# Performance work log

Hardware: AMD Instinct MI355X
Metric: run time of the kernel (lower is better)

Reference implementation:

```python
import jax, jax.numpy as jnp
import numpy as np

K = 16  # kNN size (self included)
R = 4   # upsampling ratio


def _knn(pts, k):
    # pts: (B,N,3) -> idx (B,N,k); smallest distance first, so idx[:,:,0] is self
    sq = jnp.sum(pts * pts, axis=-1)
    d = sq[:, :, None] - 2.0 * jnp.einsum('bnd,bmd->bnm', pts, pts) + sq[:, None, :]
    _, idx = jax.lax.top_k(-d, k)
    return idx


def _gather(feats, idx):
    # feats (B,N,C), idx (B,N,k) -> (B,N,k,C)
    return jax.vmap(lambda f, i: f[i])(feats, idx)


def _conv1d(x, w, b):  # pointwise Conv1d: x (B,C,N)
    return jnp.einsum('oc,bcn->bon', w, x) + b[None, :, None]


def _conv2d(x, w, b):  # pointwise Conv2d: x (B,C,N,K)
    return jnp.einsum('oc,bcnk->bonk', w, x) + b[None, :, None, None]


def setup_inputs() -> dict:
    key = jax.random.key(0)
    ks = jax.random.split(key, 16)
    B, N = 2, 8192
    w = lambda k, s: jax.random.normal(k, s, jnp.float32) * 0.1
    return {
        'x': jax.random.normal(ks[0], (B, 3, N), jnp.float32),
        'mlp1_w1': w(ks[1], (32, 3)), 'mlp1_b1': jnp.zeros((32,), jnp.float32),
        'mlp1_w2': w(ks[2], (64, 32)), 'mlp1_b2': jnp.zeros((64,), jnp.float32),
        'mlp2_w1': w(ks[3], (32, 9)), 'mlp2_b1': jnp.zeros((32,), jnp.float32),
        'mlp3_w1': w(ks[4], (128, 96)), 'mlp3_b1': jnp.zeros((128,), jnp.float32),
        'mlp3_w2': w(ks[5], (12, 128)), 'mlp3_b2': jnp.zeros((12,), jnp.float32),
        'att_w1': w(ks[6], (128, 64)), 'att_b1': jnp.zeros((128,), jnp.float32),
        'att_w2': w(ks[7], (64, 128)), 'att_b2': jnp.zeros((64,), jnp.float32),
    }


def reference(x, mlp1_w1, mlp1_b1, mlp1_w2, mlp1_b2, mlp2_w1, mlp2_b1,
              mlp3_w1, mlp3_b1, mlp3_w2, mlp3_b2,
              att_w1, att_b1, att_w2, att_b2):
    B, C, N = x.shape
    pts = jnp.transpose(x, (0, 2, 1))                     # (B,N,3)
    idx = _knn(jax.lax.stop_gradient(pts), K)             # (B,N,K)

    # local 3x3 covariance features -> (B,9,N)
    nb = _gather(pts, idx)                                # (B,N,K,3)
    c = nb - jnp.mean(nb, axis=2, keepdims=True)
    cov = jnp.einsum('bnki,bnkj->bnij', c, c) / K         # (B,N,3,3)
    cov_feat = jnp.transpose(cov.reshape(B, N, 9), (0, 2, 1))

    # mlp1: 3 -> 32 -> 64, relu on both (last_act=True)
    f1 = jax.nn.relu(_conv1d(jax.nn.relu(_conv1d(x, mlp1_w1, mlp1_b1)), mlp1_w2, mlp1_b2))

    # gather neighbor features (exclude self) and form relative features
    fk = _gather(jnp.transpose(f1, (0, 2, 1)), idx[:, :, 1:])   # (B,N,K-1,64)
    f_knn = jnp.transpose(fk, (0, 3, 1, 2)) - f1[:, :, :, None]  # (B,64,N,K-1)

    # attention MLP (2D): 64 -> 128 -> 64, softmax over neighbor axis
    h = jax.nn.relu(_conv2d(f_knn, att_w1, att_b1))
    w = jax.nn.softmax(_conv2d(h, att_w2, att_b2), axis=-1)
    f_agg = jnp.sum(w * f_knn, axis=-1)                   # (B,64,N)

    # mlp2: 9 -> 32 with relu
    f_cov = jax.nn.relu(_conv1d(cov_feat, mlp2_w1, mlp2_b1))     # (B,32,N)

    f = jnp.concatenate([f_agg, f_cov], axis=1)           # (B,96,N)
    g = _conv1d(jax.nn.relu(_conv1d(f, mlp3_w1, mlp3_b1)), mlp3_w2, mlp3_b2)  # (B,3R,N)

    return jnp.tile(x, (1, 1, R)) + 0.15 * g.reshape(B, -1, R * N)
```

## Files before the change

### kernel.cpp

```cpp
#include <hip/hip_runtime.h>

#define BB 2
#define NN 8192
#define KK 16
#define QPB 64
#define PRE2 128
#define SLICE 512
#define STASH 32
#define EPSF 0.02f
typedef unsigned long long ull;
typedef unsigned short ushort;
#define KINF 0xFFFFFFFFFFFFFFFFULL
#define BFONE 0x3F80

typedef __attribute__((ext_vector_type(8))) short short8;
typedef __attribute__((ext_vector_type(4))) float f32x4;

static __device__ __forceinline__ ushort f2bf(float f) {
    unsigned u = __float_as_uint(f);
    unsigned r = (u + 0x7FFFu + ((u >> 16) & 1u)) >> 16;
    return (ushort)r;
}
static __device__ __forceinline__ float bf2f(ushort s) {
    return __uint_as_float(((unsigned)s) << 16);
}

static __device__ __forceinline__ float distq(const float4& qp, const float4& cn) {
    return fmaf(qp.x, cn.x, fmaf(qp.y, cn.y, fmaf(qp.z, cn.z, __fadd_rn(qp.w, cn.w))));
}

__global__ __launch_bounds__(256) void prep_f1_kernel(
    const float* __restrict__ x, float4* __restrict__ pts4, float4* __restrict__ pts4n,
    ushort* __restrict__ ptsC64,
    const float* __restrict__ w1, const float* __restrict__ b1,
    const float* __restrict__ w2, const float* __restrict__ b2,
    ushort* __restrict__ f1,
    const float* __restrict__ aw1, const float* __restrict__ aw2,
    const float* __restrict__ m3w1, const float* __restrict__ m3w2,
    ushort* __restrict__ awb1, ushort* __restrict__ awb2,
    ushort* __restrict__ m3w1b, ushort* __restrict__ m3w2b)
{
    if (blockIdx.x >= 128) {
        int wt = (blockIdx.x - 128) * 256 + threadIdx.x;
        for (int c = wt; c < 7552; c += 2048) {
            int i = c * 4;
            const float* s; ushort* d; int off;
            if (i < 8192)       { s = aw1;  d = awb1;  off = i; }
            else if (i < 16384) { s = aw2;  d = awb2;  off = i - 8192; }
            else if (i < 28672) { s = m3w1; d = m3w1b; off = i - 16384; }
            else                { s = m3w2; d = m3w2b; off = i - 28672; }
            float4 v = *(const float4*)(s + off);
            ushort4 o = { f2bf(v.x), f2bf(v.y), f2bf(v.z), f2bf(v.w) };
            *(ushort4*)(d + off) = o;
        }
        return;
    }
    if (blockIdx.x < 64) {
        int t = blockIdx.x * 256 + threadIdx.x;
        int b = t >> 13, n = t & (NN - 1);
        float x0 = x[(b * 3 + 0) * NN + n];
        float x1 = x[(b * 3 + 1) * NN + n];
        float x2 = x[(b * 3 + 2) * NN + n];
        float sq = fmaf(x2, x2, fmaf(x1, x1, __fmul_rn(x0, x0)));
        pts4[t]  = make_float4(x0, x1, x2, sq);
        pts4n[t] = make_float4(-2.f * x0, -2.f * x1, -2.f * x2, sq);

        float m2x = -2.f * x0, m2y = -2.f * x1, m2z = -2.f * x2;
        ushort hx = f2bf(m2x), hy = f2bf(m2y), hz = f2bf(m2z);
        ushort lx = f2bf(m2x - bf2f(hx));
        ushort ly = f2bf(m2y - bf2f(hy));
        ushort lz = f2bf(m2z - bf2f(hz));
        ushort sh = f2bf(sq), sl = f2bf(sq - bf2f(sh));
        short8 r0 = { (short)hx, (short)hy, (short)hz, (short)lx,
                      (short)ly, (short)lz, (short)hx, (short)hy };
        short8 r1 = { (short)hz, (short)lx, (short)ly, (short)lz,
                      (short)sh, (short)sl, (short)BFONE, (short)BFONE };
        short8 zz = { 0, 0, 0, 0, 0, 0, 0, 0 };
        ushort* cp = ptsC64 + (size_t)t * 32;
        *(short8*)(cp)      = r0;
        *(short8*)(cp + 8)  = r1;
        *(short8*)(cp + 16) = zz;
        *(short8*)(cp + 24) = zz;
    } else {
        int P = (blockIdx.x - 64) * 256 + threadIdx.x;
        int b = P >> 13, n = P & (NN - 1);
        float x0 = x[(b * 3 + 0) * NN + n];
        float x1 = x[(b * 3 + 1) * NN + n];
        float x2 = x[(b * 3 + 2) * NN + n];
        float h[32];
#pragma unroll
        for (int o = 0; o < 32; ++o) {
            float v = fmaf(w1[o * 3 + 2], x2, fmaf(w1[o * 3 + 1], x1, fmaf(w1[o * 3 + 0], x0, b1[o])));
            h[o] = fmaxf(v, 0.f);
        }
#pragma unroll
        for (int o4 = 0; o4 < 16; ++o4) {
            float vv[4];
#pragma unroll
            for (int u = 0; u < 4; ++u) {
                int o = o4 * 4 + u;
                float v = b2[o];
#pragma unroll
                for (int k = 0; k < 32; ++k) v = fmaf(w2[o * 32 + k], h[k], v);
                vv[u] = fmaxf(v, 0.f);
            }
            ushort4 s = { f2bf(vv[0]), f2bf(vv[1]), f2bf(vv[2]), f2bf(vv[3]) };
            *(ushort4*)(f1 + (size_t)P * 64 + o4 * 4) = s;
        }
    }
}

#define DRAIN_TOP4()                                             \
    {                                                            \
        for (int j = 0; j < 7; ++j) {                            \
            if (!__any(j < pend)) break;                         \
            float v = pbuf[j * 1024 + t];                        \
            float k = (j < pend) ? v : 3.0e38f;                  \
            bool b3 = k < l3, b2 = k < l2, b1 = k < l1, b0 = k < l0; \
            l3 = b3 ? (b2 ? l2 : k) : l3;                        \
            l2 = b2 ? (b1 ? l1 : k) : l2;                        \
            l1 = b1 ? (b0 ? l0 : k) : l1;                        \
            l0 = b0 ? k : l0;                                    \
        }                                                        \
    }

__global__ __launch_bounds__(1024, 4) void knn_prefix_kernel(
    const float4* __restrict__ pts4, const float4* __restrict__ pts4n,
    float* __restrict__ thrb)
{
    __shared__ __align__(16) char ldsraw[61440];
    float4* stage = (float4*)ldsraw;
    float*  pbuf  = (float*)(ldsraw + 32768);
    float*  mrg   = (float*)ldsraw;

    const int t    = threadIdx.x;
    const int wv   = t >> 6;
    const int lane = t & 63;
    const int b    = blockIdx.y;
    const int q    = blockIdx.x * QPB + lane;

    const float4 qp = pts4[b * NN + q];

    {
        int f0 = t, f1 = t + 1024;
        stage[f0] = pts4n[(size_t)b * NN + ((f0 >> 7) << 9) + (f0 & 127)];
        stage[f1] = pts4n[(size_t)b * NN + ((f1 >> 7) << 9) + (f1 & 127)];
    }
    __syncthreads();

    const float4* __restrict__ cp = stage + wv * 128;

    float l0 = 3.0e38f, l1 = 3.0e38f, l2 = 3.0e38f, l3 = 3.0e38f;
    float curmax = 3.0e38f;
    int pend = 0;

#pragma unroll 1
    for (int i0 = 0; i0 < PRE2; i0 += 8) {
#pragma unroll
        for (int u = 0; u < 4; ++u) {
            float d = distq(qp, cp[i0 + u]);
            pbuf[pend * 1024 + t] = d;
            pend += (d < curmax) ? 1 : 0;
        }
        if (__any(pend >= 4)) { DRAIN_TOP4(); pend = 0; curmax = l3; }
#pragma unroll
        for (int u = 4; u < 8; ++u) {
            float d = distq(qp, cp[i0 + u]);
            pbuf[pend * 1024 + t] = d;
            pend += (d < curmax) ? 1 : 0;
        }
        if (__any(pend >= 4)) { DRAIN_TOP4(); pend = 0; curmax = l3; }
    }
    DRAIN_TOP4();

    __syncthreads();
    mrg[(wv * 4 + 0) * 64 + lane] = l0;
    mrg[(wv * 4 + 1) * 64 + lane] = l1;
    mrg[(wv * 4 + 2) * 64 + lane] = l2;
    mrg[(wv * 4 + 3) * 64 + lane] = l3;
    __syncthreads();

    if (t < QPB) {
        float h[16];
        int kc[16];
#pragma unroll
        for (int s = 0; s < 16; ++s) { h[s] = mrg[(s * 4) * 64 + t]; kc[s] = 0; }
        float best = 3.0e38f;
        for (int o = 0; o < KK; ++o) {
            best = h[0]; int bs = 0;
#pragma unroll
            for (int s = 1; s < 16; ++s) { if (h[s] < best) { best = h[s]; bs = s; } }
#pragma unroll
            for (int s = 0; s < 16; ++s) {
                if (s == bs) {
                    kc[s]++;
                    h[s] = (kc[s] < 4) ? mrg[(s * 4 + kc[s]) * 64 + t] : 3.0e38f;
                }
            }
        }
        thrb[(size_t)b * NN + blockIdx.x * QPB + t] = best;
    }
}

__global__ __launch_bounds__(256) void knn_scan_kernel(
    const float4* __restrict__ pts4, const ushort* __restrict__ ptsC64,
    const float* __restrict__ thrb, unsigned* __restrict__ bufm)
{
    __shared__ __align__(16) char lbuf[10240];

    const int t    = threadIdx.x;
    const int wv   = t >> 6;
    const int lane = t & 63;
    const int l15  = lane & 15, l4 = lane >> 4;
    const int b    = blockIdx.y;
    const int z    = blockIdx.z;
    const int qt   = blockIdx.x * 4 + wv;
    const int qbase = qt * 16;

    const float4 p = pts4[(size_t)b * NN + qbase + l15];
    const ushort qhx = f2bf(p.x), qhy = f2bf(p.y), qhz = f2bf(p.z);
    const ushort qlx = f2bf(p.x - bf2f(qhx));
    const ushort qly = f2bf(p.y - bf2f(qhy));
    const ushort qlz = f2bf(p.z - bf2f(qhz));
    const ushort qsh = f2bf(p.w), qsl = f2bf(p.w - bf2f(qsh));
    short8 qf;
    if (l4 == 0)
        qf = short8{ (short)qhx, (short)qhy, (short)qhz, (short)qhx,
                     (short)qhy, (short)qhz, (short)qlx, (short)qly };
    else if (l4 == 1)
        qf = short8{ (short)qlz, (short)qlx, (short)qly, (short)qlz,
                     (short)BFONE, (short)BFONE, (short)qsh, (short)qsl };
    else
        qf = short8{ 0, 0, 0, 0, 0, 0, 0, 0 };

    const float thrq = thrb[(size_t)b * NN + qbase + l15] * 1.001f + EPSF;

    const uint4* __restrict__ gsrc =
        (const uint4*)(ptsC64 + ((size_t)b * NN + (size_t)z * 1024) * 32);

    unsigned* __restrict__ op =
        bufm + (size_t)(b * NN + qbase + l15) * 256 + z * 32 + l4 * 8;

    uint4 r0 = gsrc[t], r1 = gsrc[t + 256];
    unsigned w4[4];

#pragma unroll 1
    for (int g = 0; g < 8; ++g) {
        __syncthreads();
        *(uint4*)(lbuf + (t >> 2) * 80 + (t & 3) * 16) = r0;
        *(uint4*)(lbuf + ((t + 256) >> 2) * 80 + (t & 3) * 16) = r1;
        if (g < 7) {
            r0 = gsrc[(g + 1) * 512 + t];
            r1 = gsrc[(g + 1) * 512 + t + 256];
        }
        __syncthreads();

        unsigned acc = 0;
#pragma unroll
        for (int i = 0; i < 8; ++i) {
            short8 cf = *(const short8*)(lbuf + (i * 16 + l15) * 80 + l4 * 16);
            f32x4 D = { 0.f, 0.f, 0.f, 0.f };
            D = __builtin_amdgcn_mfma_f32_16x16x32_bf16(cf, qf, D, 0, 0, 0);
            acc = acc * 2u + (unsigned)(D[0] <= thrq);
            acc = acc * 2u + (unsigned)(D[1] <= thrq);
            acc = acc * 2u + (unsigned)(D[2] <= thrq);
            acc = acc * 2u + (unsigned)(D[3] <= thrq);
        }
        w4[g & 3] = acc;
        if ((g & 3) == 3)
            *(uint4*)(op + (g >> 2) * 4) = make_uint4(w4[0], w4[1], w4[2], w4[3]);
    }
}

__global__ __launch_bounds__(256) void knn_select_kernel(
    const float4* __restrict__ pts4, const float4* __restrict__ pts4n,
    const unsigned* __restrict__ bufm,
    int* __restrict__ iout)
{
    __shared__ ull sm3[4][8][8][KK];
    __shared__ ushort stash[STASH][256];

    const int t = threadIdx.x;
    const int wv = t >> 6, lane = t & 63;
    const int qq = lane & 7, hh = lane >> 3;
    const int q  = (blockIdx.x * 4 + wv) * 8 + qq;
    const int b  = q >> 13;

    const float4 qp = pts4[q];
    ull list[KK];
#pragma unroll
    for (int i = 0; i < KK; ++i) list[i] = KINF;

    const unsigned* __restrict__ mrow = bufm + (size_t)q * 256 + hh * 32;
    int pend = 0;
#pragma unroll 1
    for (int g4 = 0; g4 < 8; ++g4) {
        uint4 v = ((const uint4*)mrow)[g4];
        unsigned wsv[4] = { v.x, v.y, v.z, v.w };
#pragma unroll
        for (int j = 0; j < 4; ++j) {
            unsigned w = wsv[j];
            const int W = hh * 32 + g4 * 4 + j;
            const int cb = ((W >> 5) << 10) + ((W & 7) << 7) + (((W >> 3) & 3) << 2);
            while (w) {
                int p = __builtin_ctz(w);
                w &= w - 1;
                int m = 31 - p;
                int id = cb + ((m >> 2) << 4) + (m & 3);
                if (pend < STASH) {
                    stash[pend][t] = (ushort)id;
                    ++pend;
                } else {
                    float d = distq(qp, pts4n[b * NN + id]);
                    unsigned ud = __float_as_uint(d);
                    ud ^= ((unsigned)((int)ud >> 31)) | 0x80000000u;
                    ull k = ((ull)ud << 32) | (unsigned)id;
#pragma unroll
                    for (int i2 = KK - 1; i2 > 0; --i2) {
                        bool c1 = k < list[i2];
                        bool c2 = k < list[i2 - 1];
                        ull nd = c2 ? list[i2 - 1] : k;
                        list[i2] = c1 ? nd : list[i2];
                    }
                    list[0] = (k < list[0]) ? k : list[0];
                }
            }
        }
    }

    for (int j = 0; ; j += 2) {
        if (!__any(j < pend)) break;
        int j1 = j + 1;
        int id0 = stash[(j  < pend) ? j  : 0][t];
        int id1 = stash[(j1 < pend) ? j1 : 0][t];
        float4 cn0 = pts4n[b * NN + id0];
        float4 cn1 = pts4n[b * NN + id1];

        float d0 = distq(qp, cn0);
        unsigned ud0 = __float_as_uint(d0);
        ud0 ^= ((unsigned)((int)ud0 >> 31)) | 0x80000000u;
        ull k0 = (j < pend) ? ((((ull)ud0) << 32) | (unsigned)id0) : KINF;
#pragma unroll
        for (int i2 = KK - 1; i2 > 0; --i2) {
            bool c1 = k0 < list[i2];
            bool c2 = k0 < list[i2 - 1];
            ull nd = c2 ? list[i2 - 1] : k0;
            list[i2] = c1 ? nd : list[i2];
        }
        list[0] = (k0 < list[0]) ? k0 : list[0];

        float d1 = distq(qp, cn1);
        unsigned ud1 = __float_as_uint(d1);
        ud1 ^= ((unsigned)((int)ud1 >> 31)) | 0x80000000u;
        ull k1 = (j1 < pend) ? ((((ull)ud1) << 32) | (unsigned)id1) : KINF;
#pragma unroll
        for (int i2 = KK - 1; i2 > 0; --i2) {
            bool c1 = k1 < list[i2];
            bool c2 = k1 < list[i2 - 1];
            ull nd = c2 ? list[i2 - 1] : k1;
            list[i2] = c1 ? nd : list[i2];
        }
        list[0] = (k1 < list[0]) ? k1 : list[0];
    }

#pragma unroll
    for (int k = 0; k < KK; ++k) sm3[wv][hh][qq][k] = list[k];

    if (hh == 0) {
        ull h[8]; int kc[8];
#pragma unroll
        for (int s = 0; s < 8; ++s) { h[s] = sm3[wv][s][qq][0]; kc[s] = 0; }
        int* op = iout + (size_t)q * KK;
        for (int o = 0; o < KK; ++o) {
            ull best = h[0]; int bs = 0;
#pragma unroll
            for (int s = 1; s < 8; ++s) { if (h[s] < best) { best = h[s]; bs = s; } }
            op[o] = (int)(unsigned)(best & 0xFFFFFFFFULL);
#pragma unroll
            for (int s = 0; s < 8; ++s) {
                if (s == bs) {
                    kc[s]++;
                    h[s] = (kc[s] < KK) ? sm3[wv][s][qq][kc[s]] : KINF;
                }
            }
        }
    }
}

__global__ __launch_bounds__(256, 2) void attn_cov_kernel(
    const ushort* __restrict__ f1, const int* __restrict__ idx,
    const ushort* __restrict__ awb1, const float* __restrict__ ab1,
    const ushort* __restrict__ awb2, const float* __restrict__ ab2,
    ushort* __restrict__ fagg,
    const float4* __restrict__ pts4,
    const float* __restrict__ cw, const float* __restrict__ cb,
    ushort* __restrict__ fcov)
{
    __shared__ __align__(16) ushort w1l[128][72];
    __shared__ __align__(16) ushort w2l[64][136];
    __shared__ __align__(16) ushort fkb[4][16][72];
    __shared__ __align__(16) ushort hb[4][16][136];

    const int t = threadIdx.x;

    if (blockIdx.x >= 512) {
        int P = (blockIdx.x - 512) * 256 + t;
        int b = P >> 13;
        const int4* ip4 = (const int4*)(idx + (size_t)P * KK);
        int ids[KK];
#pragma unroll
        for (int g = 0; g < 4; ++g) {
            int4 v = ip4[g];
            ids[g * 4 + 0] = v.x; ids[g * 4 + 1] = v.y;
            ids[g * 4 + 2] = v.z; ids[g * 4 + 3] = v.w;
        }
        float px[KK], py[KK], pz[KK];
#pragma unroll
        for (int k = 0; k < KK; ++k) {
            float4 c = pts4[b * NN + ids[k]];
            px[k] = c.x; py[k] = c.y; pz[k] = c.z;
        }
        float mx = 0.f, my = 0.f, mz = 0.f;
#pragma unroll
        for (int k = 0; k < KK; ++k) { mx += px[k]; my += py[k]; mz += pz[k]; }
        mx *= (1.f / 16.f); my *= (1.f / 16.f); mz *= (1.f / 16.f);
        float c00 = 0, c01 = 0, c02 = 0, c11 = 0, c12 = 0, c22 = 0;
#pragma unroll
        for (int k = 0; k < KK; ++k) {
            float dx = px[k] - mx, dy = py[k] - my, dz = pz[k] - mz;
            c00 = fmaf(dx, dx, c00); c01 = fmaf(dx, dy, c01); c02 = fmaf(dx, dz, c02);
            c11 = fmaf(dy, dy, c11); c12 = fmaf(dy, dz, c12); c22 = fmaf(dz, dz, c22);
        }
        const float inv = 1.f / 16.f;
        float cf[9] = { c00 * inv, c01 * inv, c02 * inv,
                        c01 * inv, c11 * inv, c12 * inv,
                        c02 * inv, c12 * inv, c22 * inv };
        ushort* outp = fcov + (size_t)P * 32;
#pragma unroll
        for (int o = 0; o < 32; ++o) {
            float v = cb[o];
#pragma unroll
            for (int m = 0; m < 9; ++m) v = fmaf(cw[o * 9 + m], cf[m], v);
            outp[o] = f2bf(fmaxf(v, 0.f));
        }
        return;
    }

    const int wv = t >> 6, lane = t & 63;
    const int l15 = lane & 15, qd = lane >> 4;

#pragma unroll
    for (int i = t * 8; i < 128 * 64; i += 256 * 8) {
        int r = i >> 6, c = i & 63;
        *(short8*)&w1l[r][c] = *(const short8*)(awb1 + i);
    }
#pragma unroll
    for (int i = t * 8; i < 64 * 128; i += 256 * 8) {
        int r = i >> 7, c = i & 127;
        *(short8*)&w2l[r][c] = *(const short8*)(awb2 + i);
    }
    __syncthreads();

    const int W = blockIdx.x * 4 + wv;
    for (int g = 0; g < 8; ++g) {
        const int P = W * 8 + g;
        const int b = P >> 13;

        float fc = bf2f(f1[(size_t)P * 64 + lane]);
        ushort fn[15];
#pragma unroll
        for (int j = 0; j < 15; ++j) {
            int nb = idx[(size_t)P * KK + 1 + j];
            fn[j] = f1[((size_t)b * NN + nb) * 64 + lane];
        }
#pragma unroll
        for (int j = 0; j < 15; ++j) fkb[wv][j][lane] = f2bf(bf2f(fn[j]) - fc);
        fkb[wv][15][lane] = 0;

        short8 a0 = *(const short8*)&fkb[wv][l15][qd * 8];
        short8 a1 = *(const short8*)&fkb[wv][l15][32 + qd * 8];

#pragma unroll
        for (int tile = 0; tile < 8; ++tile) {
            float bv = ab1[tile * 16 + l15];
            f32x4 acc = { bv, bv, bv, bv };
            short8 b0 = *(const short8*)&w1l[tile * 16 + l15][qd * 8];
            short8 b1f = *(const short8*)&w1l[tile * 16 + l15][32 + qd * 8];
            acc = __builtin_amdgcn_mfma_f32_16x16x32_bf16(a0, b0, acc, 0, 0, 0);
            acc = __builtin_amdgcn_mfma_f32_16x16x32_bf16(a1, b1f, acc, 0, 0, 0);
#pragma unroll
            for (int reg = 0; reg < 4; ++reg)
                hb[wv][qd * 4 + reg][tile * 16 + l15] = f2bf(fmaxf(acc[reg], 0.f));
        }

        short8 a2[4];
#pragma unroll
        for (int ks = 0; ks < 4; ++ks)
            a2[ks] = *(const short8*)&hb[wv][l15][ks * 32 + qd * 8];

        f32x4 L[4];
#pragma unroll
        for (int tile = 0; tile < 4; ++tile) {
            float bv = ab2[tile * 16 + l15];
            f32x4 acc = { bv, bv, bv, bv };
#pragma unroll
            for (int ks = 0; ks < 4; ++ks) {
                short8 bf = *(const short8*)&w2l[tile * 16 + l15][ks * 32 + qd * 8];
                acc = __builtin_amdgcn_mfma_f32_16x16x32_bf16(a2[ks], bf, acc, 0, 0, 0);
            }
            L[tile] = acc;
        }

        float fa[4];
#pragma unroll
        for (int tile = 0; tile < 4; ++tile) {
            float m1 = -3.0e38f;
#pragma unroll
            for (int reg = 0; reg < 4; ++reg)
                if (qd * 4 + reg < 15) m1 = fmaxf(m1, L[tile][reg]);
            m1 = fmaxf(m1, __shfl_xor(m1, 16));
            m1 = fmaxf(m1, __shfl_xor(m1, 32));
            float e[4], ssum = 0.f;
#pragma unroll
            for (int reg = 0; reg < 4; ++reg) {
                bool valid = (qd * 4 + reg < 15);
                e[reg] = valid ? __expf(L[tile][reg] - m1) : 0.f;
                ssum += e[reg];
            }
            ssum += __shfl_xor(ssum, 16);
            ssum += __shfl_xor(ssum, 32);
            float part = 0.f;
#pragma unroll
            for (int reg = 0; reg < 4; ++reg) {
                float fkv = bf2f(fkb[wv][qd * 4 + reg][tile * 16 + l15]);
                part = fmaf(e[reg], fkv, part);
            }
            part += __shfl_xor(part, 16);
            part += __shfl_xor(part, 32);
            fa[tile] = part / ssum;
        }
        if (qd == 0) {
#pragma unroll
            for (int tile = 0; tile < 4; ++tile)
                fagg[(size_t)P * 64 + tile * 16 + l15] = f2bf(fa[tile]);
        }
    }
}

__global__ __launch_bounds__(256) void mlp3_kernel(
    const ushort* __restrict__ fagg, const ushort* __restrict__ fcov,
    const ushort* __restrict__ w1b, const float* __restrict__ b1,
    const ushort* __restrict__ w2b, const float* __restrict__ b2,
    const float* __restrict__ x, float* __restrict__ out)
{
    __shared__ __align__(16) ushort fb[4][16][104];
    __shared__ __align__(16) ushort hb[4][16][136];

    const int t = threadIdx.x;
    const int wv = t >> 6, lane = t & 63;
    const int l15 = lane & 15, qd = lane >> 4;

    short8 w1f[8][3];
#pragma unroll
    for (int tile = 0; tile < 8; ++tile)
#pragma unroll
        for (int ks = 0; ks < 3; ++ks)
            w1f[tile][ks] = *(const short8*)(w1b + ((size_t)(tile * 16 + l15) * 96 + ks * 32 + qd * 8));
    short8 w2f[4];
#pragma unroll
    for (int ks = 0; ks < 4; ++ks) {
        short8 f = {};
        if (l15 < 12)
            f = *(const short8*)(w2b + ((size_t)l15 * 128 + ks * 32 + qd * 8));
        w2f[ks] = f;
    }

    const int T = blockIdx.x * 4 + wv;

    {
        const int pt = lane >> 2, c4 = lane & 3;
        const ushort* fap = fagg + ((size_t)(T * 16 + pt) * 64 + c4 * 16);
        *(short8*)&fb[wv][pt][c4 * 16]     = *(const short8*)(fap);
        *(short8*)&fb[wv][pt][c4 * 16 + 8] = *(const short8*)(fap + 8);
        const ushort* fcp = fcov + ((size_t)(T * 16 + pt) * 32 + c4 * 8);
        *(short8*)&fb[wv][pt][64 + c4 * 8] = *(const short8*)(fcp);
    }

    short8 a[3];
#pragma unroll
    for (int ks = 0; ks < 3; ++ks)
        a[ks] = *(const short8*)&fb[wv][l15][ks * 32 + qd * 8];

#pragma unroll
    for (int tile = 0; tile < 8; ++tile) {
        float bv = b1[tile * 16 + l15];
        f32x4 acc = { bv, bv, bv, bv };
#pragma unroll
        for (int ks = 0; ks < 3; ++ks)
            acc = __builtin_amdgcn_mfma_f32_16x16x32_bf16(a[ks], w1f[tile][ks], acc, 0, 0, 0);
#pragma unroll
        for (int reg = 0; reg < 4; ++reg)
            hb[wv][qd * 4 + reg][tile * 16 + l15] = f2bf(fmaxf(acc[reg], 0.f));
    }

    short8 a2[4];
#pragma unroll
    for (int ks = 0; ks < 4; ++ks)
        a2[ks] = *(const short8*)&hb[wv][l15][ks * 32 + qd * 8];

    float bv2 = (l15 < 12) ? b2[l15] : 0.f;
    f32x4 acc = { bv2, bv2, bv2, bv2 };
#pragma unroll
    for (int ks = 0; ks < 4; ++ks)
        acc = __builtin_amdgcn_mfma_f32_16x16x32_bf16(a2[ks], w2f[ks], acc, 0, 0, 0);

    if (l15 < 12) {
        const int c = l15 >> 2, rr = l15 & 3;
#pragma unroll
        for (int reg = 0; reg < 4; ++reg) {
            int P = T * 16 + qd * 4 + reg;
            int b = P >> 13, n = P & (NN - 1);
            float xv = x[((size_t)b * 3 + c) * NN + n];
            out[(((size_t)b * 3 + c) * 4 + rr) * NN + n] = xv + 0.15f * acc[reg];
        }
    }
}

extern "C" void kernel_launch(void* const* d_in, const int* in_sizes, int n_in,
                              void* d_out, int out_size, void* d_ws, size_t ws_size,
                              hipStream_t stream)
{
    (void)in_sizes; (void)n_in; (void)out_size; (void)ws_size;
    const float* x    = (const float*)d_in[0];
    const float* m1w1 = (const float*)d_in[1];
    const float* m1b1 = (const float*)d_in[2];
    const float* m1w2 = (const float*)d_in[3];
    const float* m1b2 = (const float*)d_in[4];
    const float* m2w1 = (const float*)d_in[5];
    const float* m2b1 = (const float*)d_in[6];
    const float* m3w1 = (const float*)d_in[7];
    const float* m3b1 = (const float*)d_in[8];
    const float* m3w2 = (const float*)d_in[9];
    const float* m3b2 = (const float*)d_in[10];
    const float* aw1  = (const float*)d_in[11];
    const float* ab1  = (const float*)d_in[12];
    const float* aw2  = (const float*)d_in[13];
    const float* ab2  = (const float*)d_in[14];
    float* out = (float*)d_out;

    char* ws = (char*)d_ws;
    float4* pts4   = (float4*)(ws + 0);
    float4* pts4n  = (float4*)(ws + 262144);
    float*  thrb   = (float*)(ws + 524288);
    int*    idxb   = (int*)  (ws + 589824);
    ushort* ptsC64 = (ushort*)(ws + 1638400);
    unsigned* bufm = (unsigned*)(ws + 2686976);
    ushort* f1b    = (ushort*)(ws + 19464192);
    ushort* fagg   = (ushort*)(ws + 21561344);
    ushort* fcov   = (ushort*)(ws + 23658496);
    ushort* awb1   = (ushort*)(ws + 24707072);
    ushort* awb2   = (ushort*)(ws + 24723456);
    ushort* m3w1b  = (ushort*)(ws + 24739840);
    ushort* m3w2b  = (ushort*)(ws + 24764416);

    prep_f1_kernel<<<136, 256, 0, stream>>>(x, pts4, pts4n, ptsC64, m1w1, m1b1, m1w2, m1b2, f1b,
                                            aw1, aw2, m3w1, m3w2, awb1, awb2, m3w1b, m3w2b);
    knn_prefix_kernel<<<dim3(NN / QPB, BB), 1024, 0, stream>>>(pts4, pts4n, thrb);
    knn_scan_kernel<<<dim3(128, BB, 8), 256, 0, stream>>>(pts4, ptsC64, thrb, bufm);
    knn_select_kernel<<<512, 256, 0, stream>>>(pts4, pts4n, bufm, idxb);
    attn_cov_kernel<<<576, 256, 0, stream>>>(f1b, idxb, awb1, ab1, awb2, ab2, fagg,
                                             pts4, m2w1, m2b1, fcov);
    mlp3_kernel<<<256, 256, 0, stream>>>(fagg, fcov, m3w1b, m3b1, m3w2b, m3b2, x, out);
}
```

Baseline: 235.3 us.

## Compute kNN threshold prefix with bf16 MFMA distances and med3 top-4 insertion

After: 223.9 us. 4.9% less time.

```diff
diff --git a/kernel.cpp b/kernel.cpp
--- a/kernel.cpp
+++ b/kernel.cpp
@@ -4,8 +4,6 @@
 #define NN 8192
 #define KK 16
 #define QPB 64
-#define PRE2 128
-#define SLICE 512
 #define STASH 32
 #define EPSF 0.02f
 typedef unsigned long long ull;
@@ -15,6 +13,12 @@
 
 typedef __attribute__((ext_vector_type(8))) short short8;
 typedef __attribute__((ext_vector_type(4))) float f32x4;
+
+#if __has_builtin(__builtin_amdgcn_fmed3f)
+#define MED3(a,b,c) __builtin_amdgcn_fmed3f((a),(b),(c))
+#else
+#define MED3(a,b,c) fmaxf(fminf((a),(b)), fminf(fmaxf((a),(b)),(c)))
+#endif
 
 static __device__ __forceinline__ ushort f2bf(float f) {
     unsigned u = __float_as_uint(f);
@@ -110,96 +114,72 @@
     }
 }
 
-#define DRAIN_TOP4()                                             \
-    {                                                            \
-        for (int j = 0; j < 7; ++j) {                            \
-            if (!__any(j < pend)) break;                         \
-            float v = pbuf[j * 1024 + t];                        \
-            float k = (j < pend) ? v : 3.0e38f;                  \
-            bool b3 = k < l3, b2 = k < l2, b1 = k < l1, b0 = k < l0; \
-            l3 = b3 ? (b2 ? l2 : k) : l3;                        \
-            l2 = b2 ? (b1 ? l1 : k) : l2;                        \
-            l1 = b1 ? (b0 ? l0 : k) : l1;                        \
-            l0 = b0 ? k : l0;                                    \
-        }                                                        \
-    }
-
-__global__ __launch_bounds__(1024, 4) void knn_prefix_kernel(
-    const float4* __restrict__ pts4, const float4* __restrict__ pts4n,
+__global__ __launch_bounds__(256) void knn_prefix_kernel(
+    const float4* __restrict__ pts4, const ushort* __restrict__ ptsC64,
     float* __restrict__ thrb)
 {
-    __shared__ __align__(16) char ldsraw[61440];
-    float4* stage = (float4*)ldsraw;
-    float*  pbuf  = (float*)(ldsraw + 32768);
-    float*  mrg   = (float*)ldsraw;
+    __shared__ __align__(16) char lbuf[10240];
 
     const int t    = threadIdx.x;
     const int wv   = t >> 6;
     const int lane = t & 63;
+    const int l15  = lane & 15, l4 = lane >> 4;
     const int b    = blockIdx.y;
-    const int q    = blockIdx.x * QPB + lane;
-
-    const float4 qp = pts4[b * NN + q];
-
-    {
-        int f0 = t, f1 = t + 1024;
-        stage[f0] = pts4n[(size_t)b * NN + ((f0 >> 7) << 9) + (f0 & 127)];
-        stage[f1] = pts4n[(size_t)b * NN + ((f1 >> 7) << 9) + (f1 & 127)];
-    }
-    __syncthreads();
-
-    const float4* __restrict__ cp = stage + wv * 128;
+    const int qbase = (blockIdx.x * 4 + wv) * 16;
+
+    const float4 p = pts4[(size_t)b * NN + qbase + l15];
+    const ushort qhx = f2bf(p.x), qhy = f2bf(p.y), qhz = f2bf(p.z);
+    const ushort qlx = f2bf(p.x - bf2f(qhx));
+    const ushort qly = f2bf(p.y - bf2f(qhy));
+    const ushort qlz = f2bf(p.z - bf2f(qhz));
+    const ushort qsh = f2bf(p.w), qsl = f2bf(p.w - bf2f(qsh));
+    short8 qf;
+    if (l4 == 0)
+        qf = short8{ (short)qhx, (short)qhy, (short)qhz, (short)qhx,
+                     (short)qhy, (short)qhz, (short)qlx, (short)qly };
+    else if (l4 == 1)
+        qf = short8{ (short)qlz, (short)qlx, (short)qly, (short)qlz,
+                     (short)BFONE, (short)BFONE, (short)qsh, (short)qsl };
+    else
+        qf = short8{ 0, 0, 0, 0, 0, 0, 0, 0 };
 
     float l0 = 3.0e38f, l1 = 3.0e38f, l2 = 3.0e38f, l3 = 3.0e38f;
-    float curmax = 3.0e38f;
-    int pend = 0;
+
+    const uint4* __restrict__ gsrc0 = (const uint4*)(ptsC64 + ((size_t)b * NN) * 32);
+    uint4 r0 = gsrc0[t], r1 = gsrc0[t + 256];
 
 #pragma unroll 1
-    for (int i0 = 0; i0 < PRE2; i0 += 8) {
-#pragma unroll
-        for (int u = 0; u < 4; ++u) {
-            float d = distq(qp, cp[i0 + u]);
-            pbuf[pend * 1024 + t] = d;
-            pend += (d < curmax) ? 1 : 0;
-        }
-        if (__any(pend >= 4)) { DRAIN_TOP4(); pend = 0; curmax = l3; }
-#pragma unroll
-        for (int u = 4; u < 8; ++u) {
-            float d = distq(qp, cp[i0 + u]);
-            pbuf[pend * 1024 + t] = d;
-            pend += (d < curmax) ? 1 : 0;
-        }
-        if (__any(pend >= 4)) { DRAIN_TOP4(); pend = 0; curmax = l3; }
-    }
-    DRAIN_TOP4();
-
-    __syncthreads();
-    mrg[(wv * 4 + 0) * 64 + lane] = l0;
-    mrg[(wv * 4 + 1) * 64 + lane] = l1;
-    mrg[(wv * 4 + 2) * 64 + lane] = l2;
-    mrg[(wv * 4 + 3) * 64 + lane] = l3;
-    __syncthreads();
-
-    if (t < QPB) {
-        float h[16];
-        int kc[16];
-#pragma unroll
-        for (int s = 0; s < 16; ++s) { h[s] = mrg[(s * 4) * 64 + t]; kc[s] = 0; }
-        float best = 3.0e38f;
-        for (int o = 0; o < KK; ++o) {
-            best = h[0]; int bs = 0;
-#pragma unroll
-            for (int s = 1; s < 16; ++s) { if (h[s] < best) { best = h[s]; bs = s; } }
-#pragma unroll
-            for (int s = 0; s < 16; ++s) {
-                if (s == bs) {
-                    kc[s]++;
-                    h[s] = (kc[s] < 4) ? mrg[(s * 4 + kc[s]) * 64 + t] : 3.0e38f;
-                }
+    for (int s = 0; s < 16; ++s) {
+        __syncthreads();
+        *(uint4*)(lbuf + (t >> 2) * 80 + (t & 3) * 16) = r0;
+        *(uint4*)(lbuf + ((t + 256) >> 2) * 80 + (t & 3) * 16) = r1;
+        if (s < 15) {
+            r0 = gsrc0[(s + 1) * 2048 + t];
+            r1 = gsrc0[(s + 1) * 2048 + t + 256];
+        }
+        __syncthreads();
+
+#pragma unroll
+        for (int i = 0; i < 8; ++i) {
+            short8 cf = *(const short8*)(lbuf + (i * 16 + l15) * 80 + l4 * 16);
+            f32x4 D = { 0.f, 0.f, 0.f, 0.f };
+            D = __builtin_amdgcn_mfma_f32_16x16x32_bf16(cf, qf, D, 0, 0, 0);
+#pragma unroll
+            for (int reg = 0; reg < 4; ++reg) {
+                float k = D[reg];
+                float n0 = fminf(l0, k);
+                float n1 = MED3(l0, l1, k);
+                float n2 = MED3(l1, l2, k);
+                float n3 = MED3(l2, l3, k);
+                l0 = n0; l1 = n1; l2 = n2; l3 = n3;
             }
         }
-        thrb[(size_t)b * NN + blockIdx.x * QPB + t] = best;
-    }
+    }
+
+    float m = l3;
+    m = fmaxf(m, __shfl_xor(m, 16));
+    m = fmaxf(m, __shfl_xor(m, 32));
+    if (l4 == 0) thrb[(size_t)b * NN + qbase + l15] = m;
 }
 
 __global__ __launch_bounds__(256) void knn_scan_kernel(
@@ -665,7 +645,7 @@
 
     prep_f1_kernel<<<136, 256, 0, stream>>>(x, pts4, pts4n, ptsC64, m1w1, m1b1, m1w2, m1b2, f1b,
                                             aw1, aw2, m3w1, m3w2, awb1, awb2, m3w1b, m3w2b);
-    knn_prefix_kernel<<<dim3(NN / QPB, BB), 1024, 0, stream>>>(pts4, pts4n, thrb);
+    knn_prefix_kernel<<<dim3(128, BB), 256, 0, stream>>>(pts4, ptsC64, thrb);
     knn_scan_kernel<<<dim3(128, BB, 8), 256, 0, stream>>>(pts4, ptsC64, thrb, bufm);
     knn_select_kernel<<<512, 256, 0, stream>>>(pts4, pts4n, bufm, idxb);
     attn_cov_kernel<<<576, 256, 0, stream>>>(f1b, idxb, awb1, ab1, awb2, ab2, fagg,
```
